# Kernel tuning notes

Measured on AMD Instinct MI355X. Metric: run time of the kernel, lower is better.

Reference implementation:

```python
import jax, jax.numpy as jnp
import numpy as np
from jax import lax

L = 1024       # sequence length
D = 64         # bond_dim
O = 128        # output_dim
P = 2          # d_phys
B = 4096       # batch
SPLIT = L // 2


def _ident(dl, dr):
    # identity boost added to every physical slice: t[k, p, k] += 1 for k < min(dl, dr)
    m = min(dl, dr)
    base = jnp.zeros((dl, dr), dtype=jnp.float32)
    base = base.at[jnp.arange(m), jnp.arange(m)].set(1.0)
    return base[:, None, :]  # (dl, 1, dr) broadcast over p


def setup_inputs() -> dict:
    key = jax.random.key(0)
    k0, k1, k2, k3, k4, k5 = jax.random.split(key, 6)
    x = jax.random.uniform(k0, (B, L), dtype=jnp.float32)
    left0 = jax.random.normal(k1, (1, P, D), dtype=jnp.float32) * 0.01 + _ident(1, D)
    left_rest = jax.random.normal(k2, (SPLIT - 1, D, P, D), dtype=jnp.float32) * 0.01 + _ident(D, D)[None]
    center = jax.random.normal(k3, (D, D, O), dtype=jnp.float32) / jnp.sqrt(jnp.float32(O))
    right_rest = jax.random.normal(k4, (L - SPLIT - 1, D, P, D), dtype=jnp.float32) * 0.01 + _ident(D, D)[None]
    right_last = jax.random.normal(k5, (D, P, 1), dtype=jnp.float32) * 0.01 + _ident(D, 1)
    return {"x": x, "left0": left0, "left_rest": left_rest, "center": center,
            "right_rest": right_rest, "right_last": right_last}


def _norm_env(env):
    return env / (jnp.linalg.norm(env, axis=1, keepdims=True) + 1e-8)


def reference(x, left0, left_rest, center, right_rest, right_last):
    angle = (jnp.pi / 2.0) * x
    phi = jnp.stack([jnp.cos(angle), jnp.sin(angle)], axis=-1)  # (B, L, P)

    # left sweep: first tensor has trivial left bond (=1)
    left = _norm_env(jnp.einsum('pr,bp->br', left0[0], phi[:, 0]))

    def lstep(env, inp):
        A, p = inp  # A: (D,P,D), p: (B,P)
        return _norm_env(jnp.einsum('bl,lpr,bp->br', env, A, p)), None

    phi_l = jnp.swapaxes(phi[:, 1:SPLIT], 0, 1)  # (SPLIT-1, B, P)
    left, _ = lax.scan(lstep, left, (left_rest, phi_l))

    # right sweep (from last site inward): last tensor has trivial right bond (=1)
    right = _norm_env(jnp.einsum('lp,bp->bl', right_last[:, :, 0], phi[:, L - 1]))

    def rstep(env, inp):
        A, p = inp
        return _norm_env(jnp.einsum('br,lpr,bp->bl', env, A, p)), None

    phi_r = jnp.swapaxes(phi[:, SPLIT:L - 1], 0, 1)[::-1]  # reversed order
    right, _ = lax.scan(rstep, right, (right_rest[::-1], phi_r))

    out = jnp.einsum('bl,br,lro->bo', left, right, center)  # (B, O)
    # F.normalize(p=2, dim=1) with eps=1e-12
    return out / jnp.clip(jnp.linalg.norm(out, axis=1, keepdims=True), 1e-12)
```

## Files before the change

### kernel.cpp

```cpp
#include <hip/hip_runtime.h>

typedef float vf4 __attribute__((ext_vector_type(4)));
typedef int vi4 __attribute__((ext_vector_type(4)));
typedef int vi2 __attribute__((ext_vector_type(2)));
typedef short short8 __attribute__((ext_vector_type(8)));
typedef unsigned short ushort8 __attribute__((ext_vector_type(8)));

#define LL 1024
#define OO 128
#define BBATCH 4096
#define NS 511
#define NP 256
#define SITE_F 8192
#define PAIR_U16 16384
#define PAIR_F 8192

__device__ __forceinline__ void gld_lds16(const float* g, float* l) {
  __builtin_amdgcn_global_load_lds(
      (const __attribute__((address_space(1))) unsigned int*)g,
      (__attribute__((address_space(3))) unsigned int*)l, 16, 0, 0);
}

__device__ __forceinline__ unsigned short f2bf(float v) {
  const unsigned uu = __builtin_bit_cast(unsigned, v);
  return (unsigned short)((uu + 0x7FFFu + ((uu >> 16) & 1u)) >> 16);
}

__global__ __launch_bounds__(256) void prep_pair(const float* __restrict__ lsrc,
                                                 const float* __restrict__ rsrc,
                                                 unsigned short* __restrict__ Wp) {
  __shared__ float X[8192];
  __shared__ float YT[8192];
  const int pair = blockIdx.x, dir = blockIdx.y;
  const int tid = threadIdx.x;
  unsigned short* dst = Wp + ((size_t)dir * NP + pair) * PAIR_U16;
  const bool ph = (pair == NP - 1);

  const float* Xg;
  const float* Yg = nullptr;
  if (dir == 0) {
    Xg = lsrc + (size_t)(2 * pair) * SITE_F;
    if (!ph) Yg = lsrc + (size_t)(2 * pair + 1) * SITE_F;
  } else {
    const int s1 = 510 - 2 * pair;
    if (!ph) {
      Xg = rsrc + (size_t)(s1 - 1) * SITE_F;
      Yg = rsrc + (size_t)s1 * SITE_F;
    } else {
      Xg = rsrc;
    }
  }
#pragma unroll
  for (int q8 = 0; q8 < 8; q8++)
    *(vf4*)&X[(q8 * 256 + tid) * 4] = *(const vf4*)&Xg[(q8 * 256 + tid) * 4];
  if (!ph) {
#pragma unroll
    for (int q8 = 0; q8 < 8; q8++) {
      const int e = (q8 * 256 + tid) * 4;
      const vf4 v = *(const vf4*)&Yg[e];
      const int A = e >> 7, B = (e >> 6) & 1, C = e & 63;
#pragma unroll
      for (int k2 = 0; k2 < 4; k2++)
        YT[(B * 64 + C + k2) * 64 + A] = v[k2];
    }
  }
  __syncthreads();

  const int kk = tid >> 2;
  const int p = (tid >> 1) & 1, q = tid & 1;
  const int s = 2 * (kk >> 4) + p;
  const int g = (kk >> 2) & 3;
  const int j = 2 * (kk & 3) + q;

  vf4 row[16];
  if (dir == 0) {
#pragma unroll
    for (int w = 0; w < 16; w++)
      row[w] = *(const vf4*)&X[kk * 128 + p * 64 + w * 4];
  } else if (!ph) {
#pragma unroll
    for (int w = 0; w < 16; w++)
      row[w] = *(const vf4*)&YT[(p * 64 + kk) * 64 + w * 4];
  }

  for (int mm = 0; mm < 64; mm++) {
    float val;
    if (dir == 0) {
      if (!ph) {
        float d = 0.f;
#pragma unroll
        for (int w = 0; w < 16; w++) {
          const vf4 y = *(const vf4*)&YT[(q * 64 + mm) * 64 + w * 4];
          d += row[w][0] * y[0] + row[w][1] * y[1] +
               row[w][2] * y[2] + row[w][3] * y[3];
        }
        val = d - ((kk == mm) ? 1.f : 0.f);
      } else {
        val = row[mm >> 2][mm & 3] - ((kk == mm) ? 1.f : 0.f);
      }
    } else {
      if (!ph) {
        float d = 0.f;
#pragma unroll
        for (int w = 0; w < 16; w++) {
          const vf4 xv = *(const vf4*)&X[mm * 128 + q * 64 + w * 4];
          d += xv[0] * row[w][0] + xv[1] * row[w][1] +
               xv[2] * row[w][2] + xv[3] * row[w][3];
        }
        val = d - ((mm == kk) ? 1.f : 0.f);
      } else {
        val = X[mm * 128 + p * 64 + kk] - ((mm == kk) ? 1.f : 0.f);
      }
    }
    const int mt = mm >> 4, c = mm & 15;
    dst[(size_t)(((mt * 8 + s) * 64) + (g << 4) + c) * 8 + j] = f2bf(val);
  }
}

__global__ __launch_bounds__(256) void prep2(const float* __restrict__ center,
                                             unsigned short* __restrict__ Cf) {
  __shared__ float S[4096];
  const int o = blockIdx.x;
  const int tid = threadIdx.x;
#pragma unroll
  for (int k = 0; k < 16; k++) {
    const int idx = k * 256 + tid;
    S[idx] = center[(size_t)idx * 128 + o];
  }
  __syncthreads();
#pragma unroll
  for (int q = 0; q < 2; q++) {
    const int slot = q * 256 + tid;
    const int lane = slot & 63, f = slot >> 6;
    const int mt = f >> 1, s = f & 1;
    const int g = lane >> 4, c = lane & 15;
    const int l = 16 * mt + c;
    ushort8 t;
#pragma unroll
    for (int j = 0; j < 8; j++) {
      const int r = 32 * s + 8 * g + j;
      t[j] = f2bf(S[l * 64 + r]);
    }
    *(ushort8*)&Cf[(size_t)((o * 8 + f) * 64 + lane) * 8] = t;
  }
}

#define STAGE_GROUP(G, BUF)                                                    \
  {                                                                            \
    _Pragma("unroll")                                                          \
    for (int s2 = 0; s2 < 2; s2++) {                                           \
      const float* src_ = Wf + (size_t)(2 * (G) + s2) * PAIR_F;                \
      float* d_ = &ring[BUF][s2][0];                                           \
      _Pragma("unroll")                                                        \
      for (int q8 = 0; q8 < 16; q8++)                                          \
        gld_lds16(src_ + q8 * 512 + tid * 4, d_ + q8 * 512 + tid * 4);         \
    }                                                                          \
  }

#define PBODY(PR, BUF, S2)                                                     \
  {                                                                            \
    const int pr_ = (PR);                                                      \
    const float* rb = &ring[BUF][S2][0];                                       \
    vf4 FC[32];                                                                \
    _Pragma("unroll")                                                          \
    for (int f = 0; f < 32; f++)                                               \
      FC[f] = *(const vf4*)&rb[f * 256 + lane * 4];                            \
    const int npr = pr_ + 1;                                                   \
    float xiN = 0.f, xjN = 0.f;                                                \
    if (npr < NP) {                                                            \
      xiN = xrow[dir ? (1022 - 2 * npr) : (1 + 2 * npr)];                      \
      xjN = (npr == NP - 1) ? 0.f                                              \
                            : xrow[dir ? (1021 - 2 * npr) : (2 + 2 * npr)];    \
    }                                                                          \
    const float keff = (ci + si) * (cj + sj);                                  \
    const float w00 = ci * cj, w01 = ci * sj;                                  \
    const float w10 = si * cj, w11 = si * sj;                                  \
    vf4 acc[4];                                                                \
    _Pragma("unroll")                                                          \
    for (int mt = 0; mt < 4; mt++) {                                           \
      vf4 z;                                                                   \
      z[0] = keff * u[mt][0]; z[1] = keff * u[mt][1];                          \
      z[2] = keff * u[mt][2]; z[3] = keff * u[mt][3];                          \
      acc[mt] = z;                                                             \
    }                                                                          \
    _Pragma("unroll")                                                          \
    for (int s = 0; s < 8; s++) {                                              \
      const float wa = (s & 1) ? w10 : w00;                                    \
      const float wb = (s & 1) ? w11 : w01;                                    \
      int pk[4];                                                               \
      _Pragma("unroll")                                                        \
      for (int t = 0; t < 4; t++) {                                            \
        const float f0 = u[s >> 1][t] * wa, f1 = u[s >> 1][t] * wb;            \
        int pp;                                                                \
        asm("v_cvt_pk_bf16_f32 %0, %1, %2" : "=v"(pp) : "v"(f0), "v"(f1));     \
        pk[t] = pp;                                                            \
      }                                                                        \
      const short8 e2s =                                                       \
          __builtin_bit_cast(short8, (vi4){pk[0], pk[1], pk[2], pk[3]});       \
      _Pragma("unroll")                                                        \
      for (int mt = 0; mt < 4; mt++)                                           \
        acc[mt] = __builtin_amdgcn_mfma_f32_16x16x32_bf16(                     \
            __builtin_bit_cast(short8, FC[mt * 8 + s]), e2s, acc[mt], 0, 0, 0);\
    }                                                                          \
    _Pragma("unroll")                                                          \
    for (int mt = 0; mt < 4; mt++) u[mt] = acc[mt];                            \
    if (npr < NP) {                                                            \
      const float qi = 0.25f * xiN, qj = 0.25f * xjN;                          \
      float c_, s_;                                                            \
      asm("v_cos_f32 %0, %1" : "=v"(c_) : "v"(qi));                            \
      asm("v_sin_f32 %0, %1" : "=v"(s_) : "v"(qi));                            \
      ci = c_; si = s_;                                                        \
      asm("v_cos_f32 %0, %1" : "=v"(c_) : "v"(qj));                            \
      asm("v_sin_f32 %0, %1" : "=v"(s_) : "v"(qj));                            \
      cj = c_; sj = s_;                                                        \
    }                                                                          \
    if ((pr_ & 3) == 3) {              \
      float nss = 0.f;                                                         \
      _Pragma("unroll")                                                        \
      for (int mt = 0; mt < 4; mt++)                                           \
        _Pragma("unroll")                                                      \
        for (int r = 0; r < 4; r++) nss += u[mt][r] * u[mt][r];                \
      nss += __shfl_xor(nss, 16);                                              \
      nss += __shfl_xor(nss, 32);                                              \
      const int eb = (__float_as_int(nss) >> 23) & 0xFF;                       \
      const float alpha = __int_as_float((127 - ((eb - 127) >> 1)) << 23);     \
      _Pragma("unroll")                                                        \
      for (int mt = 0; mt < 4; mt++)                                           \
        _Pragma("unroll")                                                      \
        for (int r = 0; r < 4; r++) u[mt][r] *= alpha;                         \
    }                                                                          \
  }

__global__ __launch_bounds__(128, 1) void sweep(const float* __restrict__ x,
                                                const float* __restrict__ left0,
                                                const float* __restrict__ right_last,
                                                const unsigned short* __restrict__ Wp,
                                                float* __restrict__ envL,
                                                float* __restrict__ envR,
                                                unsigned short* __restrict__ Rb16) {
  __shared__ float ring[2][2][PAIR_F];
  const int bid = blockIdx.x;
  const int xcd = bid & 7;
  const int dir = xcd >> 2;
  const int slot = (xcd & 3) * 32 + (bid >> 3);
  const int tid = threadIdx.x;
  const int wave = tid >> 6;
  const int lane = tid & 63;
  const int g_ = lane >> 4, c = lane & 15;
  const int b = (slot * 2 + wave) * 16 + c;
  const float* xrow = x + (size_t)b * LL;

  const float* Wf = (const float*)(Wp + (size_t)dir * NP * PAIR_U16);

  vf4 u[4];
  {
    const float x0 = xrow[dir ? (LL - 1) : 0];
    const float qrev = 0.25f * x0;
    float cs, sn;
    asm("v_cos_f32 %0, %1" : "=v"(cs) : "v"(qrev));
    asm("v_sin_f32 %0, %1" : "=v"(sn) : "v"(qrev));
#pragma unroll
    for (int mt = 0; mt < 4; mt++)
#pragma unroll
      for (int r = 0; r < 4; r++) {
        const int n = 16 * mt + 4 * g_ + r;
        const float w0 = dir ? right_last[n * 2] : left0[n];
        const float w1 = dir ? right_last[n * 2 + 1] : left0[64 + n];
        u[mt][r] = cs * w0 + sn * w1;
      }
    float ss = 0.f;
#pragma unroll
    for (int mt = 0; mt < 4; mt++)
#pragma unroll
      for (int r = 0; r < 4; r++) ss += u[mt][r] * u[mt][r];
    ss += __shfl_xor(ss, 16);
    ss += __shfl_xor(ss, 32);
    const float a0 = 1.f / (sqrtf(ss) + 1e-8f);
#pragma unroll
    for (int mt = 0; mt < 4; mt++)
#pragma unroll
      for (int r = 0; r < 4; r++) u[mt][r] *= a0;
  }

  STAGE_GROUP(0, 0)

  float ci, si, cj, sj;
  {
    const float xi = xrow[dir ? 1022 : 1];
    const float xj = xrow[dir ? 1021 : 2];
    const float qi = 0.25f * xi, qj = 0.25f * xj;
    asm("v_cos_f32 %0, %1" : "=v"(ci) : "v"(qi));
    asm("v_sin_f32 %0, %1" : "=v"(si) : "v"(qi));
    asm("v_cos_f32 %0, %1" : "=v"(cj) : "v"(qj));
    asm("v_sin_f32 %0, %1" : "=v"(sj) : "v"(qj));
  }
  __syncthreads();

  for (int g = 0; g < 128; g++) {
    const int buf = g & 1;
    if (g < 127) STAGE_GROUP(g + 1, buf ^ 1)
    PBODY(2 * g, buf, 0)
    PBODY(2 * g + 1, buf, 1)
    __syncthreads();
  }

  float nss = 0.f;
#pragma unroll
  for (int mt = 0; mt < 4; mt++)
#pragma unroll
    for (int r = 0; r < 4; r++) nss += u[mt][r] * u[mt][r];
  nss += __shfl_xor(nss, 16);
  nss += __shfl_xor(nss, 32);
  const float alpha = 1.f / (sqrtf(nss) + 1e-8f);

  float* eo = (dir ? envR : envL) + (size_t)b * 64;
#pragma unroll
  for (int mt = 0; mt < 4; mt++) {
    vf4 v;
#pragma unroll
    for (int r = 0; r < 4; r++) v[r] = u[mt][r] * alpha;
    *(vf4*)&eo[16 * mt + 4 * g_] = v;
    if (dir) {
      int p01, p23;
      asm("v_cvt_pk_bf16_f32 %0, %1, %2" : "=v"(p01) : "v"(v[0]), "v"(v[1]));
      asm("v_cvt_pk_bf16_f32 %0, %1, %2" : "=v"(p23) : "v"(v[2]), "v"(v[3]));
      *(vi2*)&Rb16[(size_t)b * 64 + 16 * mt + 4 * g_] = (vi2){p01, p23};
    }
  }
}

__global__ __launch_bounds__(256) void centerk2(const float* __restrict__ envL,
                                                const unsigned short* __restrict__ Rb16,
                                                const unsigned short* __restrict__ Cf,
                                                float* __restrict__ Pp) {
  const int b0 = blockIdx.x * 16;
  const int tid = threadIdx.x;
  const int wave = tid >> 6;
  const int lane = tid & 63;
  const int g = lane >> 4, c = lane & 15;

  short8 rf[2];
#pragma unroll
  for (int s = 0; s < 2; s++)
    rf[s] = __builtin_bit_cast(short8,
        *(const ushort8*)&Rb16[(size_t)(b0 + c) * 64 + 32 * s + 8 * g]);

  vf4 Lv[4];
#pragma unroll
  for (int mt = 0; mt < 4; mt++)
    Lv[mt] = *(const vf4*)&envL[(size_t)(b0 + c) * 64 + 16 * mt + 4 * g];

  for (int oi = 0; oi < 32; oi++) {
    const int o = wave * 32 + oi;
    const unsigned short* cb = Cf + (size_t)(o * 8) * 64 * 8;
    vf4 acc[4];
#pragma unroll
    for (int mt = 0; mt < 4; mt++) {
      const short8 a0 = __builtin_bit_cast(short8,
          *(const ushort8*)&cb[(size_t)((mt * 2 + 0) * 64 + lane) * 8]);
      const short8 a1 = __builtin_bit_cast(short8,
          *(const ushort8*)&cb[(size_t)((mt * 2 + 1) * 64 + lane) * 8]);
      vf4 z = {0.f, 0.f, 0.f, 0.f};
      z = __builtin_amdgcn_mfma_f32_16x16x32_bf16(a0, rf[0], z, 0, 0, 0);
      z = __builtin_amdgcn_mfma_f32_16x16x32_bf16(a1, rf[1], z, 0, 0, 0);
      acc[mt] = z;
    }
    float ps = 0.f;
#pragma unroll
    for (int mt = 0; mt < 4; mt++)
#pragma unroll
      for (int r = 0; r < 4; r++) ps += Lv[mt][r] * acc[mt][r];
    ps += __shfl_xor(ps, 16);
    ps += __shfl_xor(ps, 32);
    if (g == 0) Pp[(size_t)(b0 + c) * 128 + o] = ps;
  }
}

__global__ __launch_bounds__(256) void combinek2(const float* __restrict__ P,
                                                 float* __restrict__ out) {
  const int row = blockIdx.x * 8 + (threadIdx.x >> 5);
  const int o0 = (threadIdx.x & 31) * 4;
  vf4 v = *(const vf4*)&P[(size_t)row * 128 + o0];
  float ss = v[0] * v[0] + v[1] * v[1] + v[2] * v[2] + v[3] * v[3];
#pragma unroll
  for (int m = 1; m < 32; m <<= 1) ss += __shfl_xor(ss, m);
  const float inv = 1.f / fmaxf(sqrtf(ss), 1e-12f);
  v *= inv;
  *(vf4*)&out[(size_t)row * 128 + o0] = v;
}

extern "C" void kernel_launch(void* const* d_in, const int* in_sizes, int n_in,
                              void* d_out, int out_size, void* d_ws, size_t ws_size,
                              hipStream_t stream) {
  const float* x = (const float*)d_in[0];
  const float* left0 = (const float*)d_in[1];
  const float* left_rest = (const float*)d_in[2];
  const float* center = (const float*)d_in[3];
  const float* right_rest = (const float*)d_in[4];
  const float* right_last = (const float*)d_in[5];
  float* out = (float*)d_out;

  char* wsb = (char*)d_ws;
  unsigned short* Wp = (unsigned short*)wsb;
  float* envL = (float*)(Wp + (size_t)2 * NP * PAIR_U16);
  float* envR = envL + (size_t)BBATCH * 64;
  unsigned short* Rb16 = (unsigned short*)(envR + (size_t)BBATCH * 64);
  unsigned short* Cf = Rb16 + (size_t)BBATCH * 64;
  float* Pp = (float*)(Cf + (size_t)OO * 8 * 64 * 8);

  hipLaunchKernelGGL(prep_pair, dim3(NP, 2), dim3(256), 0, stream,
                     left_rest, right_rest, Wp);
  hipLaunchKernelGGL(prep2, dim3(OO), dim3(256), 0, stream, center, Cf);
  hipLaunchKernelGGL(sweep, dim3(256), dim3(128), 0, stream,
                     x, left0, right_last, Wp, envL, envR, Rb16);
  hipLaunchKernelGGL(centerk2, dim3(BBATCH / 16), dim3(256), 0, stream,
                     envL, Rb16, Cf, Pp);
  hipLaunchKernelGGL(combinek2, dim3(BBATCH / 8), dim3(256), 0, stream, Pp, out);
}
```

Measured before the change: 357.9 us.

## Split each batch chain across two waves with LDS exchange and triple-buffered staging

```diff
diff --git a/kernel.cpp b/kernel.cpp
--- a/kernel.cpp
+++ b/kernel.cpp
@@ -145,100 +145,25 @@
   }
 }
 
-#define STAGE_GROUP(G, BUF)                                                    \
+#define STAGE(P, SL)                                                           \
   {                                                                            \
+    const float* src_ = Wf + (size_t)(P) * PAIR_F;                             \
+    float* d_ = &ring[SL][0];                                                  \
     _Pragma("unroll")                                                          \
-    for (int s2 = 0; s2 < 2; s2++) {                                           \
-      const float* src_ = Wf + (size_t)(2 * (G) + s2) * PAIR_F;                \
-      float* d_ = &ring[BUF][s2][0];                                           \
-      _Pragma("unroll")                                                        \
-      for (int q8 = 0; q8 < 16; q8++)                                          \
-        gld_lds16(src_ + q8 * 512 + tid * 4, d_ + q8 * 512 + tid * 4);         \
-    }                                                                          \
-  }
-
-#define PBODY(PR, BUF, S2)                                                     \
-  {                                                                            \
-    const int pr_ = (PR);                                                      \
-    const float* rb = &ring[BUF][S2][0];                                       \
-    vf4 FC[32];                                                                \
-    _Pragma("unroll")                                                          \
-    for (int f = 0; f < 32; f++)                                               \
-      FC[f] = *(const vf4*)&rb[f * 256 + lane * 4];                            \
-    const int npr = pr_ + 1;                                                   \
-    float xiN = 0.f, xjN = 0.f;                                                \
-    if (npr < NP) {                                                            \
-      xiN = xrow[dir ? (1022 - 2 * npr) : (1 + 2 * npr)];                      \
-      xjN = (npr == NP - 1) ? 0.f                                              \
-                            : xrow[dir ? (1021 - 2 * npr) : (2 + 2 * npr)];    \
-    }                                                                          \
-    const float keff = (ci + si) * (cj + sj);                                  \
-    const float w00 = ci * cj, w01 = ci * sj;                                  \
-    const float w10 = si * cj, w11 = si * sj;                                  \
-    vf4 acc[4];                                                                \
-    _Pragma("unroll")                                                          \
-    for (int mt = 0; mt < 4; mt++) {                                           \
-      vf4 z;                                                                   \
-      z[0] = keff * u[mt][0]; z[1] = keff * u[mt][1];                          \
-      z[2] = keff * u[mt][2]; z[3] = keff * u[mt][3];                          \
-      acc[mt] = z;                                                             \
-    }                                                                          \
-    _Pragma("unroll")                                                          \
-    for (int s = 0; s < 8; s++) {                                              \
-      const float wa = (s & 1) ? w10 : w00;                                    \
-      const float wb = (s & 1) ? w11 : w01;                                    \
-      int pk[4];                                                               \
-      _Pragma("unroll")                                                        \
-      for (int t = 0; t < 4; t++) {                                            \
-        const float f0 = u[s >> 1][t] * wa, f1 = u[s >> 1][t] * wb;            \
-        int pp;                                                                \
-        asm("v_cvt_pk_bf16_f32 %0, %1, %2" : "=v"(pp) : "v"(f0), "v"(f1));     \
-        pk[t] = pp;                                                            \
-      }                                                                        \
-      const short8 e2s =                                                       \
-          __builtin_bit_cast(short8, (vi4){pk[0], pk[1], pk[2], pk[3]});       \
-      _Pragma("unroll")                                                        \
-      for (int mt = 0; mt < 4; mt++)                                           \
-        acc[mt] = __builtin_amdgcn_mfma_f32_16x16x32_bf16(                     \
-            __builtin_bit_cast(short8, FC[mt * 8 + s]), e2s, acc[mt], 0, 0, 0);\
-    }                                                                          \
-    _Pragma("unroll")                                                          \
-    for (int mt = 0; mt < 4; mt++) u[mt] = acc[mt];                            \
-    if (npr < NP) {                                                            \
-      const float qi = 0.25f * xiN, qj = 0.25f * xjN;                          \
-      float c_, s_;                                                            \
-      asm("v_cos_f32 %0, %1" : "=v"(c_) : "v"(qi));                            \
-      asm("v_sin_f32 %0, %1" : "=v"(s_) : "v"(qi));                            \
-      ci = c_; si = s_;                                                        \
-      asm("v_cos_f32 %0, %1" : "=v"(c_) : "v"(qj));                            \
-      asm("v_sin_f32 %0, %1" : "=v"(s_) : "v"(qj));                            \
-      cj = c_; sj = s_;                                                        \
-    }                                                                          \
-    if ((pr_ & 3) == 3) {              \
-      float nss = 0.f;                                                         \
-      _Pragma("unroll")                                                        \
-      for (int mt = 0; mt < 4; mt++)                                           \
-        _Pragma("unroll")                                                      \
-        for (int r = 0; r < 4; r++) nss += u[mt][r] * u[mt][r];                \
-      nss += __shfl_xor(nss, 16);                                              \
-      nss += __shfl_xor(nss, 32);                                              \
-      const int eb = (__float_as_int(nss) >> 23) & 0xFF;                       \
-      const float alpha = __int_as_float((127 - ((eb - 127) >> 1)) << 23);     \
-      _Pragma("unroll")                                                        \
-      for (int mt = 0; mt < 4; mt++)                                           \
-        _Pragma("unroll")                                                      \
-        for (int r = 0; r < 4; r++) u[mt][r] *= alpha;                         \
-    }                                                                          \
-  }
-
-__global__ __launch_bounds__(128, 1) void sweep(const float* __restrict__ x,
+    for (int q8 = 0; q8 < 8; q8++)                                             \
+      gld_lds16(src_ + q8 * 1024 + tid * 4, d_ + q8 * 1024 + tid * 4);         \
+  }
+
+__global__ __launch_bounds__(256, 1) void sweep(const float* __restrict__ x,
                                                 const float* __restrict__ left0,
                                                 const float* __restrict__ right_last,
                                                 const unsigned short* __restrict__ Wp,
                                                 float* __restrict__ envL,
                                                 float* __restrict__ envR,
                                                 unsigned short* __restrict__ Rb16) {
-  __shared__ float ring[2][2][PAIR_F];
+  __shared__ float ring[3][PAIR_F];
+  __shared__ vi4 e2x[2][2][8][64];
+  __shared__ float nssx[2][2];
   const int bid = blockIdx.x;
   const int xcd = bid & 7;
   const int dir = xcd >> 2;
@@ -246,13 +171,14 @@
   const int tid = threadIdx.x;
   const int wave = tid >> 6;
   const int lane = tid & 63;
+  const int ch = wave >> 1, h = wave & 1;
   const int g_ = lane >> 4, c = lane & 15;
-  const int b = (slot * 2 + wave) * 16 + c;
+  const int b = (slot * 2 + ch) * 16 + c;
   const float* xrow = x + (size_t)b * LL;
 
   const float* Wf = (const float*)(Wp + (size_t)dir * NP * PAIR_U16);
 
-  vf4 u[4];
+  vf4 u[2];
   {
     const float x0 = xrow[dir ? (LL - 1) : 0];
     const float qrev = 0.25f * x0;
@@ -260,71 +186,199 @@
     asm("v_cos_f32 %0, %1" : "=v"(cs) : "v"(qrev));
     asm("v_sin_f32 %0, %1" : "=v"(sn) : "v"(qrev));
 #pragma unroll
-    for (int mt = 0; mt < 4; mt++)
+    for (int lm = 0; lm < 2; lm++)
 #pragma unroll
       for (int r = 0; r < 4; r++) {
-        const int n = 16 * mt + 4 * g_ + r;
+        const int n = 16 * (2 * h + lm) + 4 * g_ + r;
         const float w0 = dir ? right_last[n * 2] : left0[n];
         const float w1 = dir ? right_last[n * 2 + 1] : left0[64 + n];
-        u[mt][r] = cs * w0 + sn * w1;
+        u[lm][r] = cs * w0 + sn * w1;
       }
     float ss = 0.f;
 #pragma unroll
-    for (int mt = 0; mt < 4; mt++)
-#pragma unroll
-      for (int r = 0; r < 4; r++) ss += u[mt][r] * u[mt][r];
+    for (int lm = 0; lm < 2; lm++)
+#pragma unroll
+      for (int r = 0; r < 4; r++) ss += u[lm][r] * u[lm][r];
     ss += __shfl_xor(ss, 16);
     ss += __shfl_xor(ss, 32);
-    const float a0 = 1.f / (sqrtf(ss) + 1e-8f);
-#pragma unroll
-    for (int mt = 0; mt < 4; mt++)
-#pragma unroll
-      for (int r = 0; r < 4; r++) u[mt][r] *= a0;
-  }
-
-  STAGE_GROUP(0, 0)
+    if (lane == 0) nssx[ch][h] = ss;
+    asm volatile("s_waitcnt lgkmcnt(0)" ::: "memory");
+    __builtin_amdgcn_sched_barrier(0);
+    __builtin_amdgcn_s_barrier();
+    const float tot = nssx[ch][0] + nssx[ch][1];
+    const float a0 = 1.f / (sqrtf(tot) + 1e-8f);
+#pragma unroll
+    for (int lm = 0; lm < 2; lm++)
+#pragma unroll
+      for (int r = 0; r < 4; r++) u[lm][r] *= a0;
+  }
 
   float ci, si, cj, sj;
   {
-    const float xi = xrow[dir ? 1022 : 1];
-    const float xj = xrow[dir ? 1021 : 2];
-    const float qi = 0.25f * xi, qj = 0.25f * xj;
+    const float qi = 0.25f * xrow[dir ? 1022 : 1];
+    const float qj = 0.25f * xrow[dir ? 1021 : 2];
     asm("v_cos_f32 %0, %1" : "=v"(ci) : "v"(qi));
     asm("v_sin_f32 %0, %1" : "=v"(si) : "v"(qi));
     asm("v_cos_f32 %0, %1" : "=v"(cj) : "v"(qj));
     asm("v_sin_f32 %0, %1" : "=v"(sj) : "v"(qj));
   }
-  __syncthreads();
-
-  for (int g = 0; g < 128; g++) {
-    const int buf = g & 1;
-    if (g < 127) STAGE_GROUP(g + 1, buf ^ 1)
-    PBODY(2 * g, buf, 0)
-    PBODY(2 * g + 1, buf, 1)
-    __syncthreads();
-  }
-
-  float nss = 0.f;
-#pragma unroll
-  for (int mt = 0; mt < 4; mt++)
-#pragma unroll
-    for (int r = 0; r < 4; r++) nss += u[mt][r] * u[mt][r];
-  nss += __shfl_xor(nss, 16);
-  nss += __shfl_xor(nss, 32);
-  const float alpha = 1.f / (sqrtf(nss) + 1e-8f);
-
-  float* eo = (dir ? envR : envL) + (size_t)b * 64;
-#pragma unroll
-  for (int mt = 0; mt < 4; mt++) {
-    vf4 v;
-#pragma unroll
-    for (int r = 0; r < 4; r++) v[r] = u[mt][r] * alpha;
-    *(vf4*)&eo[16 * mt + 4 * g_] = v;
-    if (dir) {
-      int p01, p23;
-      asm("v_cvt_pk_bf16_f32 %0, %1, %2" : "=v"(p01) : "v"(v[0]), "v"(v[1]));
-      asm("v_cvt_pk_bf16_f32 %0, %1, %2" : "=v"(p23) : "v"(v[2]), "v"(v[3]));
-      *(vi2*)&Rb16[(size_t)b * 64 + 16 * mt + 4 * g_] = (vi2){p01, p23};
+
+  STAGE(0, 0)
+  STAGE(1, 1)
+
+  vi4 e2A[4];
+  {
+    const float w00 = ci * cj, w01 = ci * sj, w10 = si * cj, w11 = si * sj;
+#pragma unroll
+    for (int k = 0; k < 4; k++) {
+      const float wa = (k & 1) ? w10 : w00;
+      const float wb = (k & 1) ? w11 : w01;
+      int pk[4];
+#pragma unroll
+      for (int t = 0; t < 4; t++) {
+        const float uv = u[k >> 1][t];
+        const float f0 = uv * wa, f1 = uv * wb;
+        int pp;
+        asm("v_cvt_pk_bf16_f32 %0, %1, %2" : "=v"(pp) : "v"(f0), "v"(f1));
+        pk[t] = pp;
+      }
+      e2A[k] = (vi4){pk[0], pk[1], pk[2], pk[3]};
+      e2x[ch][0][4 * h + k][lane] = e2A[k];
+    }
+  }
+
+  int sl = 0;
+  for (int p = 0; p < NP; p++) {
+    asm volatile("s_waitcnt lgkmcnt(0)" ::: "memory");
+    __builtin_amdgcn_sched_barrier(0);
+    __builtin_amdgcn_s_barrier();
+    const int sl2 = (sl == 0) ? 2 : (sl - 1);
+    if (p + 2 < NP) STAGE(p + 2, sl2)
+    asm volatile("s_waitcnt vmcnt(16)" ::: "memory");
+    __builtin_amdgcn_sched_barrier(0);
+
+    vf4 FC[16];
+    {
+      const float* rb = &ring[sl][0];
+#pragma unroll
+      for (int q = 0; q < 16; q++)
+        FC[q] = *(const vf4*)&rb[(16 * h + q) * 256 + lane * 4];
+    }
+    float xiN = 0.f, xjN = 0.f;
+    if (p + 1 < NP) {
+      xiN = xrow[dir ? (1022 - 2 * (p + 1)) : (1 + 2 * (p + 1))];
+      xjN = (p + 1 == NP - 1) ? 0.f
+                              : xrow[dir ? (1021 - 2 * (p + 1)) : (2 + 2 * (p + 1))];
+    }
+    vi4 eo[4];
+#pragma unroll
+    for (int k = 0; k < 4; k++) eo[k] = e2x[ch][p & 1][4 * (1 - h) + k][lane];
+
+    const float keff = (ci + si) * (cj + sj);
+    vf4 accA[2], accB[2];
+#pragma unroll
+    for (int lm = 0; lm < 2; lm++) {
+      vf4 z;
+      z[0] = keff * u[lm][0]; z[1] = keff * u[lm][1];
+      z[2] = keff * u[lm][2]; z[3] = keff * u[lm][3];
+      accA[lm] = z;
+      accB[lm] = (vf4){0.f, 0.f, 0.f, 0.f};
+    }
+#pragma unroll
+    for (int s = 0; s < 8; s++) {
+      const vi4 ев = ((s >> 2) == h) ? e2A[s & 3] : eo[s & 3];
+      const short8 e2s = __builtin_bit_cast(short8, ев);
+#pragma unroll
+      for (int lm = 0; lm < 2; lm++) {
+        if (s < 4)
+          accA[lm] = __builtin_amdgcn_mfma_f32_16x16x32_bf16(
+              __builtin_bit_cast(short8, FC[lm * 8 + s]), e2s, accA[lm], 0, 0, 0);
+        else
+          accB[lm] = __builtin_amdgcn_mfma_f32_16x16x32_bf16(
+              __builtin_bit_cast(short8, FC[lm * 8 + s]), e2s, accB[lm], 0, 0, 0);
+      }
+    }
+#pragma unroll
+    for (int lm = 0; lm < 2; lm++) u[lm] = accA[lm] + accB[lm];
+
+    if ((p & 3) == 3) {
+      float nss = 0.f;
+#pragma unroll
+      for (int lm = 0; lm < 2; lm++)
+#pragma unroll
+        for (int r = 0; r < 4; r++) nss += u[lm][r] * u[lm][r];
+      nss += __shfl_xor(nss, 16);
+      nss += __shfl_xor(nss, 32);
+      if (lane == 0) nssx[ch][h] = nss;
+    }
+    if ((p & 3) == 0 && p > 0) {
+      const float tot = nssx[ch][0] + nssx[ch][1];
+      const int eb = (__float_as_int(tot) >> 23) & 0xFF;
+      const float alpha = __int_as_float((127 - ((eb - 127) >> 1)) << 23);
+#pragma unroll
+      for (int lm = 0; lm < 2; lm++)
+#pragma unroll
+        for (int r = 0; r < 4; r++) u[lm][r] *= alpha;
+    }
+
+    if (p + 1 < NP) {
+      const float qi = 0.25f * xiN, qj = 0.25f * xjN;
+      float c_, s_;
+      asm("v_cos_f32 %0, %1" : "=v"(c_) : "v"(qi));
+      asm("v_sin_f32 %0, %1" : "=v"(s_) : "v"(qi));
+      ci = c_; si = s_;
+      asm("v_cos_f32 %0, %1" : "=v"(c_) : "v"(qj));
+      asm("v_sin_f32 %0, %1" : "=v"(s_) : "v"(qj));
+      cj = c_; sj = s_;
+      const float w00 = ci * cj, w01 = ci * sj, w10 = si * cj, w11 = si * sj;
+#pragma unroll
+      for (int k = 0; k < 4; k++) {
+        const float wa = (k & 1) ? w10 : w00;
+        const float wb = (k & 1) ? w11 : w01;
+        int pk[4];
+#pragma unroll
+        for (int t = 0; t < 4; t++) {
+          const float uv = u[k >> 1][t];
+          const float f0 = uv * wa, f1 = uv * wb;
+          int pp;
+          asm("v_cvt_pk_bf16_f32 %0, %1, %2" : "=v"(pp) : "v"(f0), "v"(f1));
+          pk[t] = pp;
+        }
+        e2A[k] = (vi4){pk[0], pk[1], pk[2], pk[3]};
+        e2x[ch][(p + 1) & 1][4 * h + k][lane] = e2A[k];
+      }
+    }
+    sl = (sl == 2) ? 0 : (sl + 1);
+  }
+
+  {
+    float nss = 0.f;
+#pragma unroll
+    for (int lm = 0; lm < 2; lm++)
+#pragma unroll
+      for (int r = 0; r < 4; r++) nss += u[lm][r] * u[lm][r];
+    nss += __shfl_xor(nss, 16);
+    nss += __shfl_xor(nss, 32);
+    if (lane == 0) nssx[ch][h] = nss;
+    asm volatile("s_waitcnt lgkmcnt(0)" ::: "memory");
+    __builtin_amdgcn_sched_barrier(0);
+    __builtin_amdgcn_s_barrier();
+    const float tot = nssx[ch][0] + nssx[ch][1];
+    const float alpha = 1.f / (sqrtf(tot) + 1e-8f);
+
+    float* eo = (dir ? envR : envL) + (size_t)b * 64;
+#pragma unroll
+    for (int lm = 0; lm < 2; lm++) {
+      vf4 v;
+#pragma unroll
+      for (int r = 0; r < 4; r++) v[r] = u[lm][r] * alpha;
+      *(vf4*)&eo[16 * (2 * h + lm) + 4 * g_] = v;
+      if (dir) {
+        int p01, p23;
+        asm("v_cvt_pk_bf16_f32 %0, %1, %2" : "=v"(p01) : "v"(v[0]), "v"(v[1]));
+        asm("v_cvt_pk_bf16_f32 %0, %1, %2" : "=v"(p23) : "v"(v[2]), "v"(v[3]));
+        *(vi2*)&Rb16[(size_t)b * 64 + 16 * (2 * h + lm) + 4 * g_] = (vi2){p01, p23};
+      }
     }
   }
 }
@@ -411,7 +465,7 @@
   hipLaunchKernelGGL(prep_pair, dim3(NP, 2), dim3(256), 0, stream,
                      left_rest, right_rest, Wp);
   hipLaunchKernelGGL(prep2, dim3(OO), dim3(256), 0, stream, center, Cf);
-  hipLaunchKernelGGL(sweep, dim3(256), dim3(128), 0, stream,
+  hipLaunchKernelGGL(sweep, dim3(256), dim3(256), 0, stream,
                      x, left0, right_last, Wp, envL, envR, Rb16);
   hipLaunchKernelGGL(centerk2, dim3(BBATCH / 16), dim3(256), 0, stream,
                      envL, Rb16, Cf, Pp);
```

After: 436.5 us. +21.9%, slower.
